# Performance work log

Hardware: AMD Instinct MI355X
Metric: run time of the kernel (lower is better)

Reference implementation:

```python
import jax, jax.numpy as jnp
import numpy as np

N, D, E_EDGES = 50000, 128, 800000
HEADS, REL_DIM, N_RELS, LAYERS = 4, 64, 64, 2
HD = HEADS * D  # per-head out_channels == d_model (concat=False)
LN_EPS = 1e-5
NEG_SLOPE = 0.2


def setup_inputs() -> dict:
    key = jax.random.key(0)
    ks = jax.random.split(key, 12)
    s = 0.02
    return {
        "x_flat": jax.random.normal(ks[0], (N, D), jnp.float32),
        "edge_index": jax.random.randint(ks[1], (2, E_EDGES), 0, N, jnp.int32),
        "edge_type": jax.random.randint(ks[2], (E_EDGES,), 0, N_RELS, jnp.int32),
        "rel_emb": jax.random.normal(ks[3], (N_RELS, REL_DIM), jnp.float32) * s,
        # stacked params for LAYERS GATv2Conv layers
        "Wl": jax.random.normal(ks[4], (LAYERS, D, HD), jnp.float32) * s,
        "bl": jnp.zeros((LAYERS, HD), jnp.float32),
        "Wr": jax.random.normal(ks[5], (LAYERS, D, HD), jnp.float32) * s,
        "br": jnp.zeros((LAYERS, HD), jnp.float32),
        "We": jax.random.normal(ks[6], (LAYERS, REL_DIM, HD), jnp.float32) * s,
        "att": jax.random.normal(ks[7], (LAYERS, HEADS, D), jnp.float32) * s,
        "b_out": jnp.zeros((LAYERS, D), jnp.float32),
        "ln_g": jnp.ones((LAYERS, D), jnp.float32),
        "ln_b": jnp.zeros((LAYERS, D), jnp.float32),
    }


def _gatv2_layer(h, src, dst, eattr, Wl, bl, Wr, br, We, att, b_out):
    # h: [N, D] -> per-head transforms [N, H, C]
    xl = (h @ Wl + bl).reshape(N, HEADS, D)   # source transform (messages)
    xr = (h @ Wr + br).reshape(N, HEADS, D)   # target transform
    xe = (eattr @ We).reshape(-1, HEADS, D)   # edge transform (no bias, PyG)
    # GATv2 attention: a^T leaky_relu(xl_j + xr_i + xe)
    s = jax.nn.leaky_relu(xl[src] + xr[dst] + xe, NEG_SLOPE)  # [E, H, C]
    logits = jnp.einsum('ehc,hc->eh', s, att)                  # [E, H]
    # segment softmax over destination nodes
    mx = jax.ops.segment_max(logits, dst, num_segments=N)      # [N, H]
    ex = jnp.exp(logits - mx[dst])
    den = jax.ops.segment_sum(ex, dst, num_segments=N)
    alpha = ex / den[dst]                                      # [E, H]
    msg = xl[src] * alpha[..., None]                           # [E, H, C]
    out = jax.ops.segment_sum(msg.reshape(-1, HD), dst, num_segments=N)
    out = out.reshape(N, HEADS, D).mean(axis=1) + b_out        # concat=False -> mean
    return out


def _layernorm(x, g, b):
    mu = x.mean(-1, keepdims=True)
    var = ((x - mu) ** 2).mean(-1, keepdims=True)
    return (x - mu) * jax.lax.rsqrt(var + LN_EPS) * g + b


def reference(x_flat, edge_index, edge_type, rel_emb, Wl, bl, Wr, br, We, att, b_out, ln_g, ln_b):
    src, dst = edge_index[0], edge_index[1]
    eattr = rel_emb[edge_type]  # [E, REL_DIM]
    h = x_flat
    for l in range(LAYERS):
        m = _gatv2_layer(h, src, dst, eattr, Wl[l], bl[l], Wr[l], br[l], We[l], att[l], b_out[l])
        m = jax.nn.gelu(m, approximate=False)  # dropout in eval mode
        h = _layernorm(h + m, ln_g[l], ln_b[l])
    return h
```

## Files before the change

kernel.cpp:

```cpp
#include <hip/hip_runtime.h>
#include <hip/hip_bf16.h>

#define NN 50000
#define DM 128
#define EE 800000
#define NH 4
#define HDIM 512
#define NRELS 64
#define RDIM 64
#define LAYERS 2

typedef short frag8 __attribute__((ext_vector_type(8)));
typedef float f32x4 __attribute__((ext_vector_type(4)));
typedef float f32x2 __attribute__((ext_vector_type(2)));

__device__ __forceinline__ float b2f(unsigned short u) {
    unsigned v = ((unsigned)u) << 16;
    union { unsigned u; float f; } c; c.u = v; return c.f;
}
__device__ __forceinline__ float b2f_lo(unsigned u) {
    union { unsigned u; float f; } c; c.u = u << 16; return c.f;
}
__device__ __forceinline__ float b2f_hi(unsigned u) {
    union { unsigned u; float f; } c; c.u = u & 0xFFFF0000u; return c.f;
}
__device__ __forceinline__ unsigned short f2b(float f) {
    union { float f; unsigned u; } c; c.f = f;
    unsigned u = c.u;
    u += 0x7FFFu + ((u >> 16) & 1u);
    return (unsigned short)(u >> 16);
}

__global__ void count_kernel(const int* __restrict__ dst, int* __restrict__ counts) {
    int e = blockIdx.x * 256 + threadIdx.x;
    if (e < EE) atomicAdd(&counts[dst[e]], 1);
}

__global__ void scan_kernel(const int* __restrict__ counts, int* __restrict__ row_ptr,
                            int* __restrict__ cursor, int n) {
    __shared__ int wsum[16];
    __shared__ int woff[17];
    int t = threadIdx.x;
    int lane = t & 63, wid = t >> 6;
    int carry = 0;
    if (t == 0) row_ptr[0] = 0;
    for (int base = 0; base < n; base += 1024) {
        int idx = base + t;
        int x = (idx < n) ? counts[idx] : 0;
        int incl = x;
        #pragma unroll
        for (int d = 1; d < 64; d <<= 1) {
            int y = __shfl_up(incl, d, 64);
            if (lane >= d) incl += y;
        }
        if (lane == 63) wsum[wid] = incl;
        __syncthreads();
        if (t == 0) {
            int s = 0;
            for (int w = 0; w < 16; ++w) { woff[w] = s; s += wsum[w]; }
            woff[16] = s;
        }
        __syncthreads();
        if (idx < n) {
            int v = carry + woff[wid] + incl;
            row_ptr[idx + 1] = v;
            cursor[idx] = v - x;
        }
        carry += woff[16];
        __syncthreads();
    }
}

__global__ void scatter_kernel(const int* __restrict__ dst, int* __restrict__ cursor,
                               int* __restrict__ perm) {
    int e = blockIdx.x * 256 + threadIdx.x;
    if (e < EE) {
        int p = atomicAdd(&cursor[dst[e]], 1);
        perm[p] = e;
    }
}

__global__ void wconv_kernel(const float* __restrict__ W, unsigned short* __restrict__ Wt) {
    int idx = blockIdx.x * 256 + threadIdx.x;
    if (idx >= DM * HDIM) return;
    int c = idx >> 7, k = idx & 127;
    Wt[idx] = f2b(W[k * HDIM + c]);
}

__global__ void hb_kernel(const float* __restrict__ h, unsigned short* __restrict__ hb, int n4) {
    int idx = blockIdx.x * 256 + threadIdx.x;
    if (idx >= n4) return;
    float4 v = ((const float4*)h)[idx];
    ushort4 o;
    o.x = f2b(v.x); o.y = f2b(v.y); o.z = f2b(v.z); o.w = f2b(v.w);
    ((ushort4*)hb)[idx] = o;
}

__global__ void xe_kernel(const float* __restrict__ rel_emb,
                          const float* __restrict__ We,
                          float* __restrict__ xef) {
    int idx = blockIdx.x * 256 + threadIdx.x;
    if (idx >= LAYERS * NRELS * HDIM) return;
    int l  = idx / (NRELS * HDIM);
    int r  = (idx / HDIM) & (NRELS - 1);
    int hc = idx & (HDIM - 1);
    const float* Wel = We + (size_t)l * RDIM * HDIM;
    float s = 0.f;
    #pragma unroll 8
    for (int d = 0; d < RDIM; ++d) s += rel_emb[r * RDIM + d] * Wel[d * HDIM + hc];
    xef[idx] = s;
}

__global__ void be_kernel(const float* __restrict__ xef, const float* __restrict__ att,
                          float* __restrict__ be) {
    int tid = blockIdx.x * 256 + threadIdx.x;
    if (tid >= LAYERS * NRELS * NH) return;
    int l = tid >> 8;
    int r = (tid >> 2) & 63;
    int hh = tid & 3;
    const float* xp = xef + (size_t)l * NRELS * HDIM + r * HDIM + hh * DM;
    const float* ap = att + (size_t)l * HDIM + hh * DM;
    float s = 0.f;
    #pragma unroll 8
    for (int c = 0; c < DM; ++c) s += ap[c] * xp[c];
    be[tid] = 0.6f * s;
}

__global__ __launch_bounds__(256) void gemm_xlxr_ab_kernel(
    const unsigned short* __restrict__ hb,
    const unsigned short* __restrict__ WtL,
    const unsigned short* __restrict__ WtR,
    const float* __restrict__ bl, const float* __restrict__ br,
    const float* __restrict__ att_l,
    unsigned short* __restrict__ xl, unsigned short* __restrict__ xr,
    float* __restrict__ ab) {
    int w = threadIdx.x >> 6, lane = threadIdx.x & 63;
    int m0 = blockIdx.x * 32;
    int colL = lane & 15, kg = lane >> 4;

    frag8 a[2][4];
    #pragma unroll
    for (int mt = 0; mt < 2; ++mt) {
        int row = m0 + mt * 16 + colL;
        if (row >= NN) row = NN - 1;
        const unsigned short* arow = hb + (size_t)row * DM;
        #pragma unroll
        for (int kc = 0; kc < 4; ++kc) {
            uint4 raw = *(const uint4*)(arow + kc * 32 + kg * 8);
            a[mt][kc] = __builtin_bit_cast(frag8, raw);
        }
    }

    float prow[2][2][4];
    #pragma unroll
    for (int mt = 0; mt < 2; ++mt)
        #pragma unroll
        for (int mat = 0; mat < 2; ++mat)
            #pragma unroll
            for (int r = 0; r < 4; ++r) prow[mt][mat][r] = 0.f;

    #pragma unroll
    for (int mat = 0; mat < 2; ++mat) {
        const unsigned short* Wt = mat ? WtR : WtL;
        const float* bias = mat ? br : bl;
        unsigned short* out = mat ? xr : xl;
        #pragma unroll
        for (int nt = 0; nt < 8; ++nt) {
            int col = w * 128 + nt * 16 + colL;
            f32x4 acc0 = {0.f, 0.f, 0.f, 0.f};
            f32x4 acc1 = {0.f, 0.f, 0.f, 0.f};
            #pragma unroll
            for (int kc = 0; kc < 4; ++kc) {
                uint4 raw = *(const uint4*)(Wt + (size_t)col * DM + kc * 32 + kg * 8);
                frag8 b = __builtin_bit_cast(frag8, raw);
                acc0 = __builtin_amdgcn_mfma_f32_16x16x32_bf16(a[0][kc], b, acc0, 0, 0, 0);
                acc1 = __builtin_amdgcn_mfma_f32_16x16x32_bf16(a[1][kc], b, acc1, 0, 0, 0);
            }
            float bb = bias[col];
            float ac = att_l[col];
            #pragma unroll
            for (int r = 0; r < 4; ++r) {
                float v0 = acc0[r] + bb;
                float v1 = acc1[r] + bb;
                int row0 = m0 + kg * 4 + r;
                int row1 = row0 + 16;
                if (row0 < NN) out[(size_t)row0 * HDIM + col] = f2b(v0);
                if (row1 < NN) out[(size_t)row1 * HDIM + col] = f2b(v1);
                prow[0][mat][r] = fmaf(ac, v0, prow[0][mat][r]);
                prow[1][mat][r] = fmaf(ac, v1, prow[1][mat][r]);
            }
        }
    }
    #pragma unroll
    for (int d = 1; d < 16; d <<= 1) {
        #pragma unroll
        for (int mt = 0; mt < 2; ++mt)
            #pragma unroll
            for (int mat = 0; mat < 2; ++mat)
                #pragma unroll
                for (int r = 0; r < 4; ++r)
                    prow[mt][mat][r] += __shfl_xor(prow[mt][mat][r], d, 64);
    }
    if (colL == 0) {
        #pragma unroll
        for (int mt = 0; mt < 2; ++mt) {
            int row = m0 + mt * 16 + kg * 4;
            #pragma unroll
            for (int mat = 0; mat < 2; ++mat)
                #pragma unroll
                for (int r = 0; r < 4; ++r)
                    if (row + r < NN)
                        ab[(size_t)(row + r) * 8 + mat * 4 + w] = 0.6f * prow[mt][mat][r];
        }
    }
}

__global__ __launch_bounds__(128) void node_fused_kernel(
    const int* __restrict__ row_ptr, const int* __restrict__ perm,
    const int* __restrict__ ei,
    const int* __restrict__ etype,
    const unsigned short* __restrict__ xl,
    const unsigned short* __restrict__ xr,
    const float* __restrict__ xef_l,
    const float* __restrict__ ab,
    const float* __restrict__ be_l,
    const float* __restrict__ att_l,
    const float* __restrict__ h_in,
    const float* __restrict__ b_out, const float* __restrict__ ln_g,
    const float* __restrict__ ln_b,
    float* __restrict__ h_out,
    unsigned short* __restrict__ hb_out) {
    int i = blockIdx.x;
    int t = threadIdx.x;
    int w = t >> 6, l = t & 63;
    int hh = l >> 4;
    __shared__ uint2 ox_l[128];
    __shared__ float cl[128][4];
    __shared__ float lsum[2][512];
    __shared__ float ssum_s[2][4];
    __shared__ float inv_s[4];
    __shared__ float red[4];

    int beg = row_ptr[i], end = row_ptr[i + 1];

    uint4 xrv = *(const uint4*)(xr + (size_t)i * HDIM + l * 8);
    f32x2 xrp[4];
    xrp[0] = f32x2{b2f_lo(xrv.x), b2f_hi(xrv.x)};
    xrp[1] = f32x2{b2f_lo(xrv.y), b2f_hi(xrv.y)};
    xrp[2] = f32x2{b2f_lo(xrv.z), b2f_hi(xrv.z)};
    xrp[3] = f32x2{b2f_lo(xrv.w), b2f_hi(xrv.w)};
    float4 at0 = ((const float4*)(att_l + l * 8))[0];
    float4 at1 = ((const float4*)(att_l + l * 8))[1];
    float atv[8] = {at0.x * 0.4f, at0.y * 0.4f, at0.z * 0.4f, at0.w * 0.4f,
                    at1.x * 0.4f, at1.y * 0.4f, at1.z * 0.4f, at1.w * 0.4f};
    float4 bxv = ((const float4*)ab)[2 * i + 1];

    const char* xl_b = (const char*)xl;
    const char* xe_b = (const char*)xef_l;
    uint l16 = (uint)l << 4, l32 = (uint)l << 5;

    float ss = 0.f;
    f32x2 acc[4];
    acc[0] = f32x2{0.f, 0.f}; acc[1] = f32x2{0.f, 0.f};
    acc[2] = f32x2{0.f, 0.f}; acc[3] = f32x2{0.f, 0.f};

    for (int cb = beg; cb < end; cb += 128) {
        int mc = min(128, end - cb);
        if (t < mc) {
            int p = perm[cb + t];
            int s = ei[p];
            int r = etype[p];
            ox_l[t].x = (uint)s << 10;
            ox_l[t].y = (uint)r << 11;
            float4 a4  = ((const float4*)ab)[2 * s];
            float4 be4 = ((const float4*)be_l)[r];
            cl[t][0] = a4.x + bxv.x + be4.x;
            cl[t][1] = a4.y + bxv.y + be4.y;
            cl[t][2] = a4.z + bxv.z + be4.z;
            cl[t][3] = a4.w + bxv.w + be4.w;
        }
        __syncthreads();
        for (int j = w; j < mc; j += 2) {
            uint2 oo = ox_l[j];
            float cj = cl[j][hh];
            uint4 vv = *(const uint4*)(xl_b + oo.x + l16);
            const float* xerow = (const float*)(xe_b + oo.y);
            float4 e0 = *(const float4*)(xerow + l * 8);
            float4 e1 = *(const float4*)(xerow + l * 8 + 4);
            f32x2 xp0 = f32x2{b2f_lo(vv.x), b2f_hi(vv.x)};
            f32x2 xp1 = f32x2{b2f_lo(vv.y), b2f_hi(vv.y)};
            f32x2 xp2 = f32x2{b2f_lo(vv.z), b2f_hi(vv.z)};
            f32x2 xp3 = f32x2{b2f_lo(vv.w), b2f_hi(vv.w)};
            f32x2 z0 = (xp0 + xrp[0]) + f32x2{e0.x, e0.y};
            f32x2 z1 = (xp1 + xrp[1]) + f32x2{e0.z, e0.w};
            f32x2 z2 = (xp2 + xrp[2]) + f32x2{e1.x, e1.y};
            f32x2 z3 = (xp3 + xrp[3]) + f32x2{e1.z, e1.w};
            float partial = fmaf(atv[0], fabsf(z0[0]),
                            fmaf(atv[1], fabsf(z0[1]),
                            fmaf(atv[2], fabsf(z1[0]),
                            fmaf(atv[3], fabsf(z1[1]),
                            fmaf(atv[4], fabsf(z2[0]),
                            fmaf(atv[5], fabsf(z2[1]),
                            fmaf(atv[6], fabsf(z3[0]), atv[7] * fabsf(z3[1]))))))));
            #pragma unroll
            for (int d = 1; d < 16; d <<= 1) partial += __shfl_xor(partial, d, 64);
            float we = __expf(partial + cj);
            ss += we;
            f32x2 wv = f32x2{we, we};
            acc[0] += wv * xp0;
            acc[1] += wv * xp1;
            acc[2] += wv * xp2;
            acc[3] += wv * xp3;
        }
        __syncthreads();
    }

    float* lw = &lsum[w][l * 8];
    lw[0] = acc[0][0]; lw[1] = acc[0][1]; lw[2] = acc[1][0]; lw[3] = acc[1][1];
    lw[4] = acc[2][0]; lw[5] = acc[2][1]; lw[6] = acc[3][0]; lw[7] = acc[3][1];
    if ((l & 15) == 0) ssum_s[w][hh] = ss;
    __syncthreads();
    if (t < 4) {
        float s = ssum_s[0][t] + ssum_s[1][t];
        inv_s[t] = (s > 0.f) ? 1.f / s : 0.f;
    }
    __syncthreads();

    int c = t;
    float o = 0.f;
    #pragma unroll
    for (int h = 0; h < 4; ++h)
        o = fmaf(lsum[0][h * 128 + c] + lsum[1][h * 128 + c], inv_s[h], o);
    o = o * 0.25f + b_out[c];
    float ge = 0.5f * o * (1.f + erff(o * 0.70710678118654752f));
    float y = h_in[(size_t)i * DM + c] + ge;

    float a = y, b = y * y;
    int lane = t & 63, wid = t >> 6;
    #pragma unroll
    for (int d = 1; d < 64; d <<= 1) {
        a += __shfl_xor(a, d, 64);
        b += __shfl_xor(b, d, 64);
    }
    if (lane == 0) { red[wid * 2 + 0] = a; red[wid * 2 + 1] = b; }
    __syncthreads();
    float mean = (red[0] + red[2]) * (1.f / 128.f);
    float var = (red[1] + red[3]) * (1.f / 128.f) - mean * mean;
    float rs = rsqrtf(var + 1e-5f);
    float out = (y - mean) * rs * ln_g[c] + ln_b[c];
    h_out[(size_t)i * DM + c] = out;
    hb_out[(size_t)i * DM + c] = f2b(out);
}

extern "C" void kernel_launch(void* const* d_in, const int* in_sizes, int n_in,
                              void* d_out, int out_size, void* d_ws, size_t ws_size,
                              hipStream_t stream) {
    const float* x_flat   = (const float*)d_in[0];
    const int*   edge_idx = (const int*)d_in[1];
    const int*   edge_ty  = (const int*)d_in[2];
    const float* rel_emb  = (const float*)d_in[3];
    const float* Wl       = (const float*)d_in[4];
    const float* bl       = (const float*)d_in[5];
    const float* Wr       = (const float*)d_in[6];
    const float* br       = (const float*)d_in[7];
    const float* We       = (const float*)d_in[8];
    const float* att      = (const float*)d_in[9];
    const float* b_out    = (const float*)d_in[10];
    const float* ln_g     = (const float*)d_in[11];
    const float* ln_b     = (const float*)d_in[12];

    char* p = (char*)d_ws;
    auto carve = [&](size_t bytes) {
        void* r = (void*)p;
        p += (bytes + 255) & ~(size_t)255;
        return r;
    };
    unsigned short* xl     = (unsigned short*)carve((size_t)NN * HDIM * 2);
    unsigned short* xr     = (unsigned short*)carve((size_t)NN * HDIM * 2);
    float*          h1     = (float*)carve((size_t)NN * DM * 4);
    unsigned short* hb     = (unsigned short*)carve((size_t)NN * DM * 2);
    unsigned short* Wt     = (unsigned short*)carve((size_t)4 * DM * HDIM * 2);
    float*          xef    = (float*)carve((size_t)LAYERS * NRELS * HDIM * 4);
    float*          ab     = (float*)carve((size_t)NN * 8 * 4);
    float*          be     = (float*)carve((size_t)LAYERS * NRELS * NH * 4);
    int*            row_ptr= (int*)carve((size_t)(NN + 1) * 4);
    int*            counts = (int*)carve((size_t)NN * 4);
    int*            cursor = (int*)carve((size_t)NN * 4);
    int*            perm   = (int*)carve((size_t)EE * 4);

    const int* dst = edge_idx + EE;

    hipMemsetAsync(counts, 0, (size_t)NN * 4, stream);
    count_kernel<<<(EE + 255) / 256, 256, 0, stream>>>(dst, counts);
    scan_kernel<<<1, 1024, 0, stream>>>(counts, row_ptr, cursor, NN);
    scatter_kernel<<<(EE + 255) / 256, 256, 0, stream>>>(dst, cursor, perm);

    for (int l = 0; l < LAYERS; ++l) {
        wconv_kernel<<<(DM * HDIM + 255) / 256, 256, 0, stream>>>(
            Wl + (size_t)l * DM * HDIM, Wt + (size_t)(l * 2 + 0) * DM * HDIM);
        wconv_kernel<<<(DM * HDIM + 255) / 256, 256, 0, stream>>>(
            Wr + (size_t)l * DM * HDIM, Wt + (size_t)(l * 2 + 1) * DM * HDIM);
    }
    xe_kernel<<<(LAYERS * NRELS * HDIM + 255) / 256, 256, 0, stream>>>(rel_emb, We, xef);
    be_kernel<<<(LAYERS * NRELS * NH + 255) / 256, 256, 0, stream>>>(xef, att, be);
    hb_kernel<<<(NN * DM / 4 + 255) / 256, 256, 0, stream>>>(x_flat, hb, NN * DM / 4);

    const float* h_cur = x_flat;
    for (int l = 0; l < LAYERS; ++l) {
        float* h_next = (l == LAYERS - 1) ? (float*)d_out : h1;
        gemm_xlxr_ab_kernel<<<(NN + 31) / 32, 256, 0, stream>>>(
            hb,
            Wt + (size_t)(l * 2 + 0) * DM * HDIM,
            Wt + (size_t)(l * 2 + 1) * DM * HDIM,
            bl + (size_t)l * HDIM, br + (size_t)l * HDIM,
            att + (size_t)l * HDIM,
            xl, xr, ab);
        node_fused_kernel<<<NN, 128, 0, stream>>>(
            row_ptr, perm, edge_idx, edge_ty, xl, xr,
            xef + (size_t)l * NRELS * HDIM,
            ab, be + (size_t)l * NRELS * NH,
            att + (size_t)l * HDIM,
            h_cur,
            b_out + (size_t)l * DM, ln_g + (size_t)l * DM, ln_b + (size_t)l * DM,
            h_next, hb);
        h_cur = h_next;
    }
}
```

Baseline: 660.7 us.

## Parallelize CSR scan, merge weight conversions, unroll edge loop by four

Replaces the single-block serial prefix scan over node degrees with a three-kernel multi-block scan (block sums, scan of sums, finalize). Merges the four weight transpose/convert launches into one kernel. In the node kernel, each wave now handles a contiguous half of the edge chunk and processes four edges per iteration, issuing all gathers before the math to raise memory-level parallelism. The cost is more registers per thread in the node kernel and two extra launches for the scan.

```diff
diff --git a/kernel.cpp b/kernel.cpp
--- a/kernel.cpp
+++ b/kernel.cpp
@@ -9,6 +9,7 @@
 #define NRELS 64
 #define RDIM 64
 #define LAYERS 2
+#define NB 196
 
 typedef short frag8 __attribute__((ext_vector_type(8)));
 typedef float f32x4 __attribute__((ext_vector_type(4)));
@@ -36,38 +37,62 @@
     if (e < EE) atomicAdd(&counts[dst[e]], 1);
 }
 
-__global__ void scan_kernel(const int* __restrict__ counts, int* __restrict__ row_ptr,
-                            int* __restrict__ cursor, int n) {
-    __shared__ int wsum[16];
-    __shared__ int woff[17];
+__global__ __launch_bounds__(256) void psum_kernel(const int* __restrict__ counts,
+                                                   int* __restrict__ psums) {
+    int idx = blockIdx.x * 256 + threadIdx.x;
+    int x = (idx < NN) ? counts[idx] : 0;
+    int lane = threadIdx.x & 63, wv = threadIdx.x >> 6;
+    #pragma unroll
+    for (int d = 1; d < 64; d <<= 1) x += __shfl_xor(x, d, 64);
+    __shared__ int ws[4];
+    if (lane == 0) ws[wv] = x;
+    __syncthreads();
+    if (threadIdx.x == 0) psums[blockIdx.x] = ws[0] + ws[1] + ws[2] + ws[3];
+}
+
+__global__ __launch_bounds__(256) void pscan_kernel(const int* __restrict__ psums,
+                                                    int* __restrict__ offs,
+                                                    int* __restrict__ row_ptr) {
     int t = threadIdx.x;
-    int lane = t & 63, wid = t >> 6;
-    int carry = 0;
+    int x = (t < NB) ? psums[t] : 0;
+    int lane = t & 63, wv = t >> 6;
+    int incl = x;
+    #pragma unroll
+    for (int d = 1; d < 64; d <<= 1) {
+        int y = __shfl_up(incl, d, 64);
+        if (lane >= d) incl += y;
+    }
+    __shared__ int ws[4];
+    if (lane == 63) ws[wv] = incl;
+    __syncthreads();
+    int off = 0;
+    for (int k = 0; k < wv; ++k) off += ws[k];
+    if (t < NB) offs[t] = incl + off - x;
     if (t == 0) row_ptr[0] = 0;
-    for (int base = 0; base < n; base += 1024) {
-        int idx = base + t;
-        int x = (idx < n) ? counts[idx] : 0;
-        int incl = x;
-        #pragma unroll
-        for (int d = 1; d < 64; d <<= 1) {
-            int y = __shfl_up(incl, d, 64);
-            if (lane >= d) incl += y;
-        }
-        if (lane == 63) wsum[wid] = incl;
-        __syncthreads();
-        if (t == 0) {
-            int s = 0;
-            for (int w = 0; w < 16; ++w) { woff[w] = s; s += wsum[w]; }
-            woff[16] = s;
-        }
-        __syncthreads();
-        if (idx < n) {
-            int v = carry + woff[wid] + incl;
-            row_ptr[idx + 1] = v;
-            cursor[idx] = v - x;
-        }
-        carry += woff[16];
-        __syncthreads();
+}
+
+__global__ __launch_bounds__(256) void pfin_kernel(const int* __restrict__ counts,
+                                                   const int* __restrict__ offs,
+                                                   int* __restrict__ row_ptr,
+                                                   int* __restrict__ cursor) {
+    int idx = blockIdx.x * 256 + threadIdx.x;
+    int x = (idx < NN) ? counts[idx] : 0;
+    int lane = threadIdx.x & 63, wv = threadIdx.x >> 6;
+    int incl = x;
+    #pragma unroll
+    for (int d = 1; d < 64; d <<= 1) {
+        int y = __shfl_up(incl, d, 64);
+        if (lane >= d) incl += y;
+    }
+    __shared__ int ws[4];
+    if (lane == 63) ws[wv] = incl;
+    __syncthreads();
+    int off = offs[blockIdx.x];
+    for (int k = 0; k < wv; ++k) off += ws[k];
+    if (idx < NN) {
+        int v = off + incl;
+        row_ptr[idx + 1] = v;
+        cursor[idx] = v - x;
     }
 }
 
@@ -80,11 +105,16 @@
     }
 }
 
-__global__ void wconv_kernel(const float* __restrict__ W, unsigned short* __restrict__ Wt) {
+__global__ void wconv_all_kernel(const float* __restrict__ Wl, const float* __restrict__ Wr,
+                                 unsigned short* __restrict__ Wt) {
     int idx = blockIdx.x * 256 + threadIdx.x;
-    if (idx >= DM * HDIM) return;
-    int c = idx >> 7, k = idx & 127;
-    Wt[idx] = f2b(W[k * HDIM + c]);
+    if (idx >= 4 * DM * HDIM) return;
+    int m = idx >> 16;
+    int r = idx & 65535;
+    int c = r >> 7, k = r & 127;
+    int l = m >> 1;
+    const float* W = (m & 1) ? Wr : Wl;
+    Wt[idx] = f2b(W[(size_t)l * DM * HDIM + k * HDIM + c]);
 }
 
 __global__ void hb_kernel(const float* __restrict__ h, unsigned short* __restrict__ hb, int n4) {
@@ -215,6 +245,39 @@
     }
 }
 
+#define EDGE_LOAD(k, jj)                                              \
+    uint2 oo##k = ox_l[jj];                                           \
+    float cj##k = cl[jj][hh];                                         \
+    uint4 vv##k = *(const uint4*)(xl_b + oo##k.x + l16);              \
+    float4 e0##k = *(const float4*)(xe_b + oo##k.y + l32);            \
+    float4 e1##k = *(const float4*)(xe_b + oo##k.y + l32 + 16);
+
+#define EDGE_PROC(k) {                                                \
+    f32x2 xp0 = f32x2{b2f_lo(vv##k.x), b2f_hi(vv##k.x)};              \
+    f32x2 xp1 = f32x2{b2f_lo(vv##k.y), b2f_hi(vv##k.y)};              \
+    f32x2 xp2 = f32x2{b2f_lo(vv##k.z), b2f_hi(vv##k.z)};              \
+    f32x2 xp3 = f32x2{b2f_lo(vv##k.w), b2f_hi(vv##k.w)};              \
+    f32x2 z0 = (xp0 + xrp0) + f32x2{e0##k.x, e0##k.y};                \
+    f32x2 z1 = (xp1 + xrp1) + f32x2{e0##k.z, e0##k.w};                \
+    f32x2 z2 = (xp2 + xrp2) + f32x2{e1##k.x, e1##k.y};                \
+    f32x2 z3 = (xp3 + xrp3) + f32x2{e1##k.z, e1##k.w};                \
+    float partial = fmaf(atv[0], fabsf(z0[0]),                        \
+                    fmaf(atv[1], fabsf(z0[1]),                        \
+                    fmaf(atv[2], fabsf(z1[0]),                        \
+                    fmaf(atv[3], fabsf(z1[1]),                        \
+                    fmaf(atv[4], fabsf(z2[0]),                        \
+                    fmaf(atv[5], fabsf(z2[1]),                        \
+                    fmaf(atv[6], fabsf(z3[0]), atv[7] * fabsf(z3[1])))))))); \
+    _Pragma("unroll")                                                 \
+    for (int d = 1; d < 16; d <<= 1) partial += __shfl_xor(partial, d, 64); \
+    float we = __expf(partial + cj##k);                               \
+    ss += we;                                                         \
+    f32x2 wv = f32x2{we, we};                                         \
+    acc0v += wv * xp0;                                                \
+    acc1v += wv * xp1;                                                \
+    acc2v += wv * xp2;                                                \
+    acc3v += wv * xp3; }
+
 __global__ __launch_bounds__(128) void node_fused_kernel(
     const int* __restrict__ row_ptr, const int* __restrict__ perm,
     const int* __restrict__ ei,
@@ -244,11 +307,10 @@
     int beg = row_ptr[i], end = row_ptr[i + 1];
 
     uint4 xrv = *(const uint4*)(xr + (size_t)i * HDIM + l * 8);
-    f32x2 xrp[4];
-    xrp[0] = f32x2{b2f_lo(xrv.x), b2f_hi(xrv.x)};
-    xrp[1] = f32x2{b2f_lo(xrv.y), b2f_hi(xrv.y)};
-    xrp[2] = f32x2{b2f_lo(xrv.z), b2f_hi(xrv.z)};
-    xrp[3] = f32x2{b2f_lo(xrv.w), b2f_hi(xrv.w)};
+    f32x2 xrp0 = f32x2{b2f_lo(xrv.x), b2f_hi(xrv.x)};
+    f32x2 xrp1 = f32x2{b2f_lo(xrv.y), b2f_hi(xrv.y)};
+    f32x2 xrp2 = f32x2{b2f_lo(xrv.z), b2f_hi(xrv.z)};
+    f32x2 xrp3 = f32x2{b2f_lo(xrv.w), b2f_hi(xrv.w)};
     float4 at0 = ((const float4*)(att_l + l * 8))[0];
     float4 at1 = ((const float4*)(att_l + l * 8))[1];
     float atv[8] = {at0.x * 0.4f, at0.y * 0.4f, at0.z * 0.4f, at0.w * 0.4f,
@@ -260,9 +322,8 @@
     uint l16 = (uint)l << 4, l32 = (uint)l << 5;
 
     float ss = 0.f;
-    f32x2 acc[4];
-    acc[0] = f32x2{0.f, 0.f}; acc[1] = f32x2{0.f, 0.f};
-    acc[2] = f32x2{0.f, 0.f}; acc[3] = f32x2{0.f, 0.f};
+    f32x2 acc0v = f32x2{0.f, 0.f}, acc1v = f32x2{0.f, 0.f};
+    f32x2 acc2v = f32x2{0.f, 0.f}, acc3v = f32x2{0.f, 0.f};
 
     for (int cb = beg; cb < end; cb += 128) {
         int mc = min(128, end - cb);
@@ -280,44 +341,30 @@
             cl[t][3] = a4.w + bxv.w + be4.w;
         }
         __syncthreads();
-        for (int j = w; j < mc; j += 2) {
-            uint2 oo = ox_l[j];
-            float cj = cl[j][hh];
-            uint4 vv = *(const uint4*)(xl_b + oo.x + l16);
-            const float* xerow = (const float*)(xe_b + oo.y);
-            float4 e0 = *(const float4*)(xerow + l * 8);
-            float4 e1 = *(const float4*)(xerow + l * 8 + 4);
-            f32x2 xp0 = f32x2{b2f_lo(vv.x), b2f_hi(vv.x)};
-            f32x2 xp1 = f32x2{b2f_lo(vv.y), b2f_hi(vv.y)};
-            f32x2 xp2 = f32x2{b2f_lo(vv.z), b2f_hi(vv.z)};
-            f32x2 xp3 = f32x2{b2f_lo(vv.w), b2f_hi(vv.w)};
-            f32x2 z0 = (xp0 + xrp[0]) + f32x2{e0.x, e0.y};
-            f32x2 z1 = (xp1 + xrp[1]) + f32x2{e0.z, e0.w};
-            f32x2 z2 = (xp2 + xrp[2]) + f32x2{e1.x, e1.y};
-            f32x2 z3 = (xp3 + xrp[3]) + f32x2{e1.z, e1.w};
-            float partial = fmaf(atv[0], fabsf(z0[0]),
-                            fmaf(atv[1], fabsf(z0[1]),
-                            fmaf(atv[2], fabsf(z1[0]),
-                            fmaf(atv[3], fabsf(z1[1]),
-                            fmaf(atv[4], fabsf(z2[0]),
-                            fmaf(atv[5], fabsf(z2[1]),
-                            fmaf(atv[6], fabsf(z3[0]), atv[7] * fabsf(z3[1]))))))));
-            #pragma unroll
-            for (int d = 1; d < 16; d <<= 1) partial += __shfl_xor(partial, d, 64);
-            float we = __expf(partial + cj);
-            ss += we;
-            f32x2 wv = f32x2{we, we};
-            acc[0] += wv * xp0;
-            acc[1] += wv * xp1;
-            acc[2] += wv * xp2;
-            acc[3] += wv * xp3;
+        int half = mc >> 1;
+        int jb = w ? half : 0;
+        int je = w ? mc : half;
+        int j = jb;
+        for (; j + 4 <= je; j += 4) {
+            EDGE_LOAD(0, j)
+            EDGE_LOAD(1, j + 1)
+            EDGE_LOAD(2, j + 2)
+            EDGE_LOAD(3, j + 3)
+            EDGE_PROC(0)
+            EDGE_PROC(1)
+            EDGE_PROC(2)
+            EDGE_PROC(3)
+        }
+        for (; j < je; ++j) {
+            EDGE_LOAD(0, j)
+            EDGE_PROC(0)
         }
         __syncthreads();
     }
 
     float* lw = &lsum[w][l * 8];
-    lw[0] = acc[0][0]; lw[1] = acc[0][1]; lw[2] = acc[1][0]; lw[3] = acc[1][1];
-    lw[4] = acc[2][0]; lw[5] = acc[2][1]; lw[6] = acc[3][0]; lw[7] = acc[3][1];
+    lw[0] = acc0v[0]; lw[1] = acc0v[1]; lw[2] = acc1v[0]; lw[3] = acc1v[1];
+    lw[4] = acc2v[0]; lw[5] = acc2v[1]; lw[6] = acc3v[0]; lw[7] = acc3v[1];
     if ((l & 15) == 0) ssum_s[w][hh] = ss;
     __syncthreads();
     if (t < 4) {
@@ -387,20 +434,19 @@
     int*            counts = (int*)carve((size_t)NN * 4);
     int*            cursor = (int*)carve((size_t)NN * 4);
     int*            perm   = (int*)carve((size_t)EE * 4);
+    int*            psums  = (int*)carve((size_t)NB * 4);
+    int*            offs   = (int*)carve((size_t)NB * 4);
 
     const int* dst = edge_idx + EE;
 
     hipMemsetAsync(counts, 0, (size_t)NN * 4, stream);
     count_kernel<<<(EE + 255) / 256, 256, 0, stream>>>(dst, counts);
-    scan_kernel<<<1, 1024, 0, stream>>>(counts, row_ptr, cursor, NN);
+    psum_kernel<<<NB, 256, 0, stream>>>(counts, psums);
+    pscan_kernel<<<1, 256, 0, stream>>>(psums, offs, row_ptr);
+    pfin_kernel<<<NB, 256, 0, stream>>>(counts, offs, row_ptr, cursor);
     scatter_kernel<<<(EE + 255) / 256, 256, 0, stream>>>(dst, cursor, perm);
 
-    for (int l = 0; l < LAYERS; ++l) {
-        wconv_kernel<<<(DM * HDIM + 255) / 256, 256, 0, stream>>>(
-            Wl + (size_t)l * DM * HDIM, Wt + (size_t)(l * 2 + 0) * DM * HDIM);
-        wconv_kernel<<<(DM * HDIM + 255) / 256, 256, 0, stream>>>(
-            Wr + (size_t)l * DM * HDIM, Wt + (size_t)(l * 2 + 1) * DM * HDIM);
-    }
+    wconv_all_kernel<<<(4 * DM * HDIM + 255) / 256, 256, 0, stream>>>(Wl, Wr, Wt);
     xe_kernel<<<(LAYERS * NRELS * HDIM + 255) / 256, 256, 0, stream>>>(rel_emb, We, xef);
     be_kernel<<<(LAYERS * NRELS * NH + 255) / 256, 256, 0, stream>>>(xef, att, be);
     hb_kernel<<<(NN * DM / 4 + 255) / 256, 256, 0, stream>>>(x_flat, hb, NN * DM / 4);
```

Measured after the change: 641.2 us. 1.03x faster.
